# Performance work log

Hardware: AMD Instinct MI355X
Metric: run time of the kernel (lower is better)

Reference implementation:

```python
import jax, jax.numpy as jnp
import numpy as np
import math

EMB = 128
HW = 128

def setup_inputs() -> dict:
    key = jax.random.key(0)
    k_t, k1, k2, k3, k4 = jax.random.split(key, 5)
    B = 8192
    t = jax.random.uniform(k_t, (B,), dtype=jnp.float32)
    s = 1.0 / math.sqrt(EMB)
    W1 = jax.random.uniform(k1, (EMB, EMB), dtype=jnp.float32, minval=-s, maxval=s)
    b1 = jax.random.uniform(k2, (EMB,), dtype=jnp.float32, minval=-s, maxval=s)
    W2 = jax.random.uniform(k3, (EMB, EMB), dtype=jnp.float32, minval=-s, maxval=s)
    b2 = jax.random.uniform(k4, (EMB,), dtype=jnp.float32, minval=-s, maxval=s)
    return {"t": t, "W1": W1, "b1": b1, "W2": W2, "b2": b2}

def reference(t, W1, b1, W2, b2):
    # sinusoidal embedding: 64 log-spaced freqs in [1, 1000]
    freqs = jnp.exp(jnp.linspace(math.log(1.0), math.log(1000.0), EMB // 2)).astype(jnp.float32)
    ang = (2.0 * math.pi) * freqs  # [64]
    phase = t[:, None] * ang[None, :]  # [B, 64]
    emb = jnp.concatenate([jnp.sin(phase), jnp.cos(phase)], axis=-1)  # [B, 128]
    # MLP: Linear -> SiLU -> Linear -> SiLU (torch Linear: x @ W.T + b)
    h = jax.nn.silu(emb @ W1.T + b1)
    h = jax.nn.silu(h @ W2.T + b2)
    # [B,1,1,128] nearest-upsampled to [B,1,128,128]: broadcast along H
    out = jnp.broadcast_to(h[:, None, None, :], (h.shape[0], 1, HW, HW))
    return out
```

## Files before the change

kernel.cpp:

```cpp
#include <hip/hip_runtime.h>
#include <math.h>

typedef float f32x4 __attribute__((ext_vector_type(4)));

__global__ __launch_bounds__(256) void k_fused(
    const float* __restrict__ t,
    const float* __restrict__ W1, const float* __restrict__ b1,
    const float* __restrict__ W2, const float* __restrict__ b2,
    float* __restrict__ out)
{
    __shared__ __attribute__((aligned(16))) float4 WQ[4096];
    __shared__ __attribute__((aligned(16))) float  EH[8 * 128];
    __shared__ __attribute__((aligned(16))) float  H1[8 * 128];

    const int tid  = threadIdx.x;
    const int base = blockIdx.x * 8;

    const int r  = tid & 127;
    const int g  = tid >> 7;
    const int xr = r & 31;

    {
        const float4* gp = (const float4*)W1;
        #pragma unroll
        for (int it = 0; it < 16; ++it) {
            int idx4 = it * 256 + tid;
            float4 q = gp[idx4];
            int rr = idx4 >> 5, c = idx4 & 31;
            WQ[rr * 32 + (c ^ (rr & 31))] = q;
        }
    }
    #pragma unroll
    for (int i = 0; i < 2; ++i) {
        int idx = i * 256 + tid;
        int b = idx >> 6, k = idx & 63;
        double a   = (double)k * (6.907755278982137 / 63.0);
        float freq = (float)exp(a);
        float ang  = 6.2831853071795865f * freq;
        float ph   = t[base + b] * ang;
        float sv, cv;
        sincosf(ph, &sv, &cv);
        EH[b * 128 + k]      = sv;
        EH[b * 128 + 64 + k] = cv;
    }
    __syncthreads();

    {
        float acc[4];
        float bv = b1[r];
        #pragma unroll
        for (int m = 0; m < 4; ++m) acc[m] = bv;
        #pragma unroll
        for (int k4 = 0; k4 < 32; ++k4) {
            float4 w = WQ[r * 32 + (k4 ^ xr)];
            #pragma unroll
            for (int m = 0; m < 4; ++m) {
                float4 ev = ((const float4*)(EH + (g * 4 + m) * 128))[k4];
                acc[m] = fmaf(w.x, ev.x, acc[m]);
                acc[m] = fmaf(w.y, ev.y, acc[m]);
                acc[m] = fmaf(w.z, ev.z, acc[m]);
                acc[m] = fmaf(w.w, ev.w, acc[m]);
            }
        }
        #pragma unroll
        for (int m = 0; m < 4; ++m) {
            float a = acc[m];
            H1[(g * 4 + m) * 128 + r] = a / (1.0f + expf(-a));
        }
    }
    __syncthreads();

    {
        const float4* gp = (const float4*)W2;
        #pragma unroll
        for (int it = 0; it < 16; ++it) {
            int idx4 = it * 256 + tid;
            float4 q = gp[idx4];
            int rr = idx4 >> 5, c = idx4 & 31;
            WQ[rr * 32 + (c ^ (rr & 31))] = q;
        }
    }
    __syncthreads();

    {
        float acc[4];
        float bv = b2[r];
        #pragma unroll
        for (int m = 0; m < 4; ++m) acc[m] = bv;
        #pragma unroll
        for (int k4 = 0; k4 < 32; ++k4) {
            float4 w = WQ[r * 32 + (k4 ^ xr)];
            #pragma unroll
            for (int m = 0; m < 4; ++m) {
                float4 ev = ((const float4*)(H1 + (g * 4 + m) * 128))[k4];
                acc[m] = fmaf(w.x, ev.x, acc[m]);
                acc[m] = fmaf(w.y, ev.y, acc[m]);
                acc[m] = fmaf(w.z, ev.z, acc[m]);
                acc[m] = fmaf(w.w, ev.w, acc[m]);
            }
        }
        #pragma unroll
        for (int m = 0; m < 4; ++m) {
            float a = acc[m];
            EH[(g * 4 + m) * 128 + r] = a / (1.0f + expf(-a));
        }
    }
    __syncthreads();

    #pragma unroll
    for (int m = 0; m < 8; ++m) {
        f32x4 v = *(const f32x4*)&EH[m * 128 + (tid & 31) * 4];
        f32x4* d = (f32x4*)(out + (size_t)(base + m) * 16384);
        #pragma unroll
        for (int c = 0; c < 16; ++c) {
            d[c * 256 + tid] = v;
        }
    }
}

extern "C" void kernel_launch(void* const* d_in, const int* in_sizes, int n_in,
                              void* d_out, int out_size, void* d_ws, size_t ws_size,
                              hipStream_t stream) {
    const float* t  = (const float*)d_in[0];
    const float* W1 = (const float*)d_in[1];
    const float* b1 = (const float*)d_in[2];
    const float* W2 = (const float*)d_in[3];
    const float* b2 = (const float*)d_in[4];
    float* out = (float*)d_out;
    const int B = in_sizes[0];

    k_fused<<<B / 8, 256, 0, stream>>>(t, W1, b1, W2, b2, out);
}
```

Measured before the change: 539.0 us.

## Read MLP weights directly from global/L2 instead of staging in LDS

Drops the 64KB shared-memory staging of W1 and W2, along with the XOR swizzle and one barrier. Each thread now reads its weight row straight from global memory (cached in L2/L1), and the launch bounds request 4 blocks per CU. The goal is to remove the per-block 128KB weight copy through LDS and raise occupancy so the output-write-bound kernel overlaps better. The cost is uncoalesced strided row reads from cache, since each thread reads a different 512B row per step.

```diff
diff --git a/kernel.cpp b/kernel.cpp
--- a/kernel.cpp
+++ b/kernel.cpp
@@ -3,33 +3,21 @@
 
 typedef float f32x4 __attribute__((ext_vector_type(4)));
 
-__global__ __launch_bounds__(256) void k_fused(
+__global__ __launch_bounds__(256, 4) void k_fused(
     const float* __restrict__ t,
     const float* __restrict__ W1, const float* __restrict__ b1,
     const float* __restrict__ W2, const float* __restrict__ b2,
     float* __restrict__ out)
 {
-    __shared__ __attribute__((aligned(16))) float4 WQ[4096];
-    __shared__ __attribute__((aligned(16))) float  EH[8 * 128];
-    __shared__ __attribute__((aligned(16))) float  H1[8 * 128];
+    __shared__ __attribute__((aligned(16))) float EH[8 * 128];
+    __shared__ __attribute__((aligned(16))) float H1[8 * 128];
 
     const int tid  = threadIdx.x;
     const int base = blockIdx.x * 8;
 
-    const int r  = tid & 127;
-    const int g  = tid >> 7;
-    const int xr = r & 31;
+    const int r = tid & 127;
+    const int g = tid >> 7;
 
-    {
-        const float4* gp = (const float4*)W1;
-        #pragma unroll
-        for (int it = 0; it < 16; ++it) {
-            int idx4 = it * 256 + tid;
-            float4 q = gp[idx4];
-            int rr = idx4 >> 5, c = idx4 & 31;
-            WQ[rr * 32 + (c ^ (rr & 31))] = q;
-        }
-    }
     #pragma unroll
     for (int i = 0; i < 2; ++i) {
         int idx = i * 256 + tid;
@@ -46,16 +34,17 @@
     __syncthreads();
 
     {
+        const f32x4* wp = (const f32x4*)(W1 + r * 128);
         float acc[4];
         float bv = b1[r];
         #pragma unroll
         for (int m = 0; m < 4; ++m) acc[m] = bv;
-        #pragma unroll
+        #pragma unroll 4
         for (int k4 = 0; k4 < 32; ++k4) {
-            float4 w = WQ[r * 32 + (k4 ^ xr)];
+            f32x4 w = wp[k4];
             #pragma unroll
             for (int m = 0; m < 4; ++m) {
-                float4 ev = ((const float4*)(EH + (g * 4 + m) * 128))[k4];
+                f32x4 ev = ((const f32x4*)(EH + (g * 4 + m) * 128))[k4];
                 acc[m] = fmaf(w.x, ev.x, acc[m]);
                 acc[m] = fmaf(w.y, ev.y, acc[m]);
                 acc[m] = fmaf(w.z, ev.z, acc[m]);
@@ -71,28 +60,17 @@
     __syncthreads();
 
     {
-        const float4* gp = (const float4*)W2;
-        #pragma unroll
-        for (int it = 0; it < 16; ++it) {
-            int idx4 = it * 256 + tid;
-            float4 q = gp[idx4];
-            int rr = idx4 >> 5, c = idx4 & 31;
-            WQ[rr * 32 + (c ^ (rr & 31))] = q;
-        }
-    }
-    __syncthreads();
-
-    {
+        const f32x4* wp = (const f32x4*)(W2 + r * 128);
         float acc[4];
         float bv = b2[r];
         #pragma unroll
         for (int m = 0; m < 4; ++m) acc[m] = bv;
-        #pragma unroll
+        #pragma unroll 4
         for (int k4 = 0; k4 < 32; ++k4) {
-            float4 w = WQ[r * 32 + (k4 ^ xr)];
+            f32x4 w = wp[k4];
             #pragma unroll
             for (int m = 0; m < 4; ++m) {
-                float4 ev = ((const float4*)(H1 + (g * 4 + m) * 128))[k4];
+                f32x4 ev = ((const f32x4*)(H1 + (g * 4 + m) * 128))[k4];
                 acc[m] = fmaf(w.x, ev.x, acc[m]);
                 acc[m] = fmaf(w.y, ev.y, acc[m]);
                 acc[m] = fmaf(w.z, ev.z, acc[m]);
```

After: 555.5 us. +3.1%, slower.
